# Performance work log

Hardware: AMD Instinct MI355X
Metric: run time of the kernel (lower is better)

## Reference

```python
import jax, jax.numpy as jnp
import numpy as np

N, E, F, H, C = 100000, 1600000, 128, 128, 40


def setup_inputs() -> dict:
    key = jax.random.key(0)
    ks = jax.random.split(key, 9)
    feat = jax.random.normal(ks[0], (N, F), dtype=jnp.float32)
    src = jax.random.randint(ks[1], (E,), 0, N, dtype=jnp.int32)
    dst = jax.random.randint(ks[2], (E,), 0, N, dtype=jnp.int32)
    def glorot(k, fan_in, fan_out):
        s = np.float32(np.sqrt(6.0 / (fan_in + fan_out)))
        return jax.random.uniform(k, (fan_in, fan_out), jnp.float32, -s, s)
    W0 = glorot(ks[3], F, H); b0 = jnp.zeros((H,), jnp.float32)
    W1 = glorot(ks[4], H, H); b1 = jnp.zeros((H,), jnp.float32)
    W2 = glorot(ks[5], H, C); b2 = jnp.zeros((C,), jnp.float32)
    return {"feat": feat, "src": src, "dst": dst,
            "W0": W0, "b0": b0, "W1": W1, "b1": b1, "W2": W2, "b2": b2}


def _graph_conv(h, src, dst, norm_out, norm_in, W, b):
    # DGL GraphConv, norm='both': out = D_in^{-1/2} A D_out^{-1/2} h W + b
    h = h * norm_out[:, None]          # scale by source out-degree
    h = h @ W                          # transform first (in_dim >= out_dim path)
    agg = jax.ops.segment_sum(h[src], dst, num_segments=N)  # scatter-add over edges
    return agg * norm_in[:, None] + b


def reference(feat, src, dst, W0, b0, W1, b1, W2, b2):
    ones_e = jnp.ones((E,), jnp.float32)
    deg_out = jax.ops.segment_sum(ones_e, src, num_segments=N)
    deg_in = jax.ops.segment_sum(ones_e, dst, num_segments=N)
    norm_out = jnp.where(deg_out > 0, jax.lax.rsqrt(jnp.maximum(deg_out, 1.0)), 0.0)
    norm_in = jnp.where(deg_in > 0, jax.lax.rsqrt(jnp.maximum(deg_in, 1.0)), 0.0)
    h = _graph_conv(feat, src, dst, norm_out, norm_in, W0, b0)
    h = jax.nn.relu(h)
    h = _graph_conv(h, src, dst, norm_out, norm_in, W1, b1)
    h = jax.nn.relu(h)
    h = _graph_conv(h, src, dst, norm_out, norm_in, W2, b2)
    return h
```

## Files before the change

### kernel.cpp

```cpp
#include <hip/hip_runtime.h>


#define KDIM 128
#define EPB 4096

typedef __attribute__((ext_vector_type(4))) float f32x4;
typedef __attribute__((ext_vector_type(8))) short short8;

__device__ __forceinline__ float bf2f(unsigned short u) {
    unsigned int x = ((unsigned int)u) << 16;
    return __builtin_bit_cast(float, x);
}
__device__ __forceinline__ unsigned short f2bf(float f) {
    unsigned int x = __builtin_bit_cast(unsigned int, f);
    unsigned int r = x + 0x7FFFu + ((x >> 16) & 1u);
    return (unsigned short)(r >> 16);
}

__global__ __launch_bounds__(256) void b0_count(const int* __restrict__ src,
                                                const int* __restrict__ dst,
                                                int* __restrict__ gcntA,
                                                int* __restrict__ gcntB, int E, int nb) {
    __shared__ int hA[512], hB[512];
    const int t = threadIdx.x;
    for (int b = t; b < nb; b += 256) { hA[b] = 0; hB[b] = 0; }
    __syncthreads();
    const int base = blockIdx.x * EPB;
#pragma unroll
    for (int i = 0; i < 16; ++i) {
        int e = base + i * 256 + t;
        if (e < E) {
            atomicAdd(&hA[dst[e] >> 8], 1);
            atomicAdd(&hB[src[e] >> 8], 1);
        }
    }
    __syncthreads();
    for (int b = t; b < nb; b += 256) {
        if (hA[b]) atomicAdd(&gcntA[b], hA[b]);
        if (hB[b]) atomicAdd(&gcntB[b], hB[b]);
    }
}

__global__ __launch_bounds__(512) void b0b_offsets(const int* __restrict__ gcntA,
                                                   const int* __restrict__ gcntB,
                                                   int* __restrict__ offA,
                                                   int* __restrict__ offB,
                                                   int* __restrict__ gcurA,
                                                   int* __restrict__ gcurB,
                                                   int* __restrict__ row_off,
                                                   int nb, int N, int E) {
    __shared__ int sm[512];
    const int t = threadIdx.x;
    int v = (t < nb) ? gcntA[t] : 0;
    sm[t] = v;
    __syncthreads();
    for (int o = 1; o < 512; o <<= 1) {
        int x = (t >= o) ? sm[t - o] : 0;
        __syncthreads();
        sm[t] += x;
        __syncthreads();
    }
    if (t < nb) { offA[t + 1] = sm[t]; gcurA[t] = sm[t] - v; }
    if (t == 0) { offA[0] = 0; row_off[N] = E; }
    __syncthreads();
    int vb = (t < nb) ? gcntB[t] : 0;
    sm[t] = vb;
    __syncthreads();
    for (int o = 1; o < 512; o <<= 1) {
        int x = (t >= o) ? sm[t - o] : 0;
        __syncthreads();
        sm[t] += x;
        __syncthreads();
    }
    if (t < nb) { offB[t + 1] = sm[t]; gcurB[t] = sm[t] - vb; }
    if (t == 0) offB[0] = 0;
}

__global__ __launch_bounds__(256) void b1_bin(const int* __restrict__ src,
                                              const int* __restrict__ dst,
                                              int* __restrict__ gcurA,
                                              int* __restrict__ gcurB,
                                              int* __restrict__ binA,
                                              int* __restrict__ binB, int E, int nb) {
    __shared__ int hA[512], hB[512];
    const int t = threadIdx.x;
    for (int b = t; b < nb; b += 256) { hA[b] = 0; hB[b] = 0; }
    __syncthreads();
    const int base = blockIdx.x * EPB;
    int se[16], de[16];
#pragma unroll
    for (int i = 0; i < 16; ++i) {
        int e = base + i * 256 + t;
        se[i] = -1; de[i] = 0;
        if (e < E) {
            se[i] = src[e]; de[i] = dst[e];
            atomicAdd(&hA[de[i] >> 8], 1);
            atomicAdd(&hB[se[i] >> 8], 1);
        }
    }
    __syncthreads();
    for (int b = t; b < nb; b += 256) {
        int c = hA[b];
        hA[b] = c ? atomicAdd(&gcurA[b], c) : 0;
        c = hB[b];
        hB[b] = c ? atomicAdd(&gcurB[b], c) : 0;
    }
    __syncthreads();
#pragma unroll
    for (int i = 0; i < 16; ++i) {
        if (se[i] >= 0) {
            int pA = atomicAdd(&hA[de[i] >> 8], 1);
            binA[pA] = se[i] | ((de[i] & 255) << 17);
            int pB = atomicAdd(&hB[se[i] >> 8], 1);
            binB[pB] = se[i] & 255;
        }
    }
}

__global__ __launch_bounds__(256) void b2_final(const int* __restrict__ binA,
                                                const int* __restrict__ binB,
                                                const int* __restrict__ offA,
                                                const int* __restrict__ offB,
                                                int* __restrict__ ssrc,
                                                int* __restrict__ row_off,
                                                float* __restrict__ norm_in,
                                                int* __restrict__ degO, int N) {
    __shared__ int h[256], cur[256];
    const int b = blockIdx.x, t = threadIdx.x;
    const int nA0 = offA[b], cntA = offA[b + 1] - nA0;
    const int nodes = min(256, N - b * 256);

    h[t] = 0;
    __syncthreads();
    for (int k = t; k < cntA; k += 256) atomicAdd(&h[binA[nA0 + k] >> 17], 1);
    __syncthreads();

    int v = h[t];
    cur[t] = v;
    __syncthreads();
    for (int o = 1; o < 256; o <<= 1) {
        int x = (t >= o) ? cur[t - o] : 0;
        __syncthreads();
        cur[t] += x;
        __syncthreads();
    }
    const int rbase = nA0 + (cur[t] - v);
    if (t < nodes) {
        row_off[b * 256 + t] = rbase;
        norm_in[b * 256 + t] = (v > 0) ? rsqrtf((float)v) : 0.0f;
    }
    __syncthreads();
    cur[t] = rbase;
    __syncthreads();

    for (int k = t; k < cntA; k += 256) {
        int val = binA[nA0 + k];
        int pos = atomicAdd(&cur[val >> 17], 1);
        ssrc[pos] = val & 0x1FFFF;
    }

    __syncthreads();
    h[t] = 0;
    __syncthreads();
    const int nB0 = offB[b], cntB = offB[b + 1] - nB0;
    for (int k = t; k < cntB; k += 256) atomicAdd(&h[binB[nB0 + k]], 1);
    __syncthreads();
    if (t < nodes) degO[b * 256 + t] = h[t];
}

__global__ __launch_bounds__(256) void prep_w(const float* __restrict__ W,
                                              unsigned int* __restrict__ Wtg) {
    int idx = blockIdx.x * 256 + threadIdx.x;
    if (idx < 8192) {
        int c = idx >> 6, kk = idx & 63;
        unsigned short lo = f2bf(W[(2 * kk) * 128 + c]);
        unsigned short hi = f2bf(W[(2 * kk + 1) * 128 + c]);
        Wtg[idx] = (unsigned)lo | ((unsigned)hi << 16);
    }
}

__global__ __launch_bounds__(256, 4) void gemm_mfma(const float* __restrict__ X,
                                                    const int* __restrict__ degO,
                                                    const unsigned int* __restrict__ Wtg,
                                                    unsigned short* __restrict__ Tb,
                                                    int ntiles, int gridWaves) {
    __shared__ unsigned int Wt[128 * 68];
    const int t = threadIdx.x;
    for (int idx = t; idx < 128 * 64; idx += 256) {
        int c = idx >> 6, kk = idx & 63;
        Wt[c * 68 + kk] = Wtg[idx];
    }
    __syncthreads();

    const int lane = t & 63;
    const int w = t >> 6;
    const int l15 = lane & 15;
    const int lh = lane >> 4;
    const unsigned short* Wts = reinterpret_cast<const unsigned short*>(Wt);
    const float4* X4 = reinterpret_cast<const float4*>(X);

    for (int tile = blockIdx.x * 4 + w; tile < ntiles; tile += gridWaves) {
        const int row = tile * 16 + l15;
        const int dv = degO[row];
        const float s = (dv > 0) ? rsqrtf((float)dv) : 0.0f;
        const float4* Xr = X4 + ((size_t)row * 32 + lh * 2);

        f32x4 acc[8];
#pragma unroll
        for (int ct = 0; ct < 8; ++ct) acc[ct] = f32x4{0.f, 0.f, 0.f, 0.f};

#pragma unroll
        for (int kc = 0; kc < 4; ++kc) {
            float4 a0 = Xr[kc * 8];
            float4 a1 = Xr[kc * 8 + 1];
            short8 af;
            af[0] = (short)f2bf(a0.x * s); af[1] = (short)f2bf(a0.y * s);
            af[2] = (short)f2bf(a0.z * s); af[3] = (short)f2bf(a0.w * s);
            af[4] = (short)f2bf(a1.x * s); af[5] = (short)f2bf(a1.y * s);
            af[6] = (short)f2bf(a1.z * s); af[7] = (short)f2bf(a1.w * s);
            const int k0 = kc * 32 + lh * 8;
#pragma unroll
            for (int ct = 0; ct < 8; ++ct) {
                short8 bf = *reinterpret_cast<const short8*>(&Wts[(ct * 16 + l15) * 136 + k0]);
                acc[ct] = __builtin_amdgcn_mfma_f32_16x16x32_bf16(af, bf, acc[ct], 0, 0, 0);
            }
        }

        const int rbase = tile * 16 + lh * 4;
#pragma unroll
        for (int ct = 0; ct < 8; ++ct) {
            const int col = ct * 16 + l15;
#pragma unroll
            for (int r = 0; r < 4; ++r)
                Tb[(size_t)(rbase + r) * 128 + col] = f2bf(acc[ct][r]);
        }
    }
}

__global__ __launch_bounds__(256) void agg_bf16(const unsigned short* __restrict__ Tb,
                                                const int* __restrict__ row_off,
                                                const int* __restrict__ ssrc,
                                                const float* __restrict__ norm_in,
                                                const float* __restrict__ bias,
                                                float* __restrict__ out, int n) {
    const int wid = (int)((blockIdx.x * blockDim.x + threadIdx.x) >> 6);
    const int lane = threadIdx.x & 63;
    if (wid >= n) return;
    const uint* T2 = reinterpret_cast<const uint*>(Tb);
    const int e0 = row_off[wid], e1 = row_off[wid + 1];
    float ax = 0.f, ay = 0.f;
    int e = e0;
    for (; e + 4 <= e1; e += 4) {
        int s0 = ssrc[e], s1 = ssrc[e + 1], s2 = ssrc[e + 2], s3 = ssrc[e + 3];
        uint v0 = T2[(size_t)s0 * 64 + lane];
        uint v1 = T2[(size_t)s1 * 64 + lane];
        uint v2 = T2[(size_t)s2 * 64 + lane];
        uint v3 = T2[(size_t)s3 * 64 + lane];
        ax += bf2f((unsigned short)v0) + bf2f((unsigned short)v1)
            + bf2f((unsigned short)v2) + bf2f((unsigned short)v3);
        ay += bf2f((unsigned short)(v0 >> 16)) + bf2f((unsigned short)(v1 >> 16))
            + bf2f((unsigned short)(v2 >> 16)) + bf2f((unsigned short)(v3 >> 16));
    }
    for (; e < e1; ++e) {
        uint v = T2[(size_t)ssrc[e] * 64 + lane];
        ax += bf2f((unsigned short)v);
        ay += bf2f((unsigned short)(v >> 16));
    }
    float ni = norm_in[wid];
    float2 b = reinterpret_cast<const float2*>(bias)[lane];
    float ox = fmaxf(ax * ni + b.x, 0.f);
    float oy = fmaxf(ay * ni + b.y, 0.f);
    reinterpret_cast<float2*>(out)[(size_t)wid * 64 + lane] = make_float2(ox, oy);
}

template <int M, int RPB, int CPT>
__global__ __launch_bounds__(256) void gemm_scaled(const float* __restrict__ X,
                                                   const int* __restrict__ degO,
                                                   const float* __restrict__ W,
                                                   float* __restrict__ T, int nrows) {
    constexpr int CG = M / CPT;
    static_assert(CG * (RPB / 2) == 256, "thread mapping");
    __shared__ float xs[KDIM][RPB + 1];
    __shared__ float ws[64][M];

    const int t = threadIdx.x;
    const int rowbase = blockIdx.x * RPB;

    {
        constexpr int NV = RPB * (KDIM / 4) / 256;
        const float4* X4 = reinterpret_cast<const float4*>(X);
#pragma unroll
        for (int i = 0; i < NV; ++i) {
            int idx = t + i * 256;
            int rl = idx >> 5;
            int kq = idx & 31;
            int row = rowbase + rl;
            float4 v = make_float4(0.f, 0.f, 0.f, 0.f);
            float s = 0.f;
            if (row < nrows) {
                v = X4[(size_t)row * 32 + kq];
                int dv = degO[row];
                s = (dv > 0) ? rsqrtf((float)dv) : 0.0f;
            }
            xs[4 * kq + 0][rl] = v.x * s;
            xs[4 * kq + 1][rl] = v.y * s;
            xs[4 * kq + 2][rl] = v.z * s;
            xs[4 * kq + 3][rl] = v.w * s;
        }
    }

    const int rg = t / CG, cg = t % CG;
    const int r0 = 2 * rg, cb = cg * CPT;
    float acc0[CPT] = {0.f}, acc1[CPT] = {0.f};

    for (int kc = 0; kc < 2; ++kc) {
        __syncthreads();
        {
            constexpr int TOT4 = 64 * M / 4;
            const float4* W4 = reinterpret_cast<const float4*>(W);
            for (int i = t; i < TOT4; i += 256) {
                int kk = i / (M / 4), m4 = i % (M / 4);
                float4 v = W4[(size_t)(kc * 64 + kk) * (M / 4) + m4];
                ws[kk][4 * m4 + 0] = v.x;
                ws[kk][4 * m4 + 1] = v.y;
                ws[kk][4 * m4 + 2] = v.z;
                ws[kk][4 * m4 + 3] = v.w;
            }
        }
        __syncthreads();
#pragma unroll 8
        for (int k = 0; k < 64; ++k) {
            float xv0 = xs[kc * 64 + k][r0];
            float xv1 = xs[kc * 64 + k][r0 + 1];
#pragma unroll
            for (int j = 0; j < CPT; ++j) {
                float wv = ws[k][cb + j];
                acc0[j] = fmaf(xv0, wv, acc0[j]);
                acc1[j] = fmaf(xv1, wv, acc1[j]);
            }
        }
    }

    int row0 = rowbase + r0;
    if (row0 < nrows) {
#pragma unroll
        for (int j = 0; j < CPT; ++j) T[(size_t)row0 * M + cb + j] = acc0[j];
    }
    if (row0 + 1 < nrows) {
#pragma unroll
        for (int j = 0; j < CPT; ++j) T[(size_t)(row0 + 1) * M + cb + j] = acc1[j];
    }
}

template <int M, bool RELU>
__global__ __launch_bounds__(256) void agg_kernel(const float* __restrict__ T,
                                                  const int* __restrict__ row_off,
                                                  const int* __restrict__ ssrc,
                                                  const float* __restrict__ norm_in,
                                                  const float* __restrict__ bias,
                                                  float* __restrict__ out, int n) {
    const int wid = (int)((blockIdx.x * blockDim.x + threadIdx.x) >> 6);
    const int lane = threadIdx.x & 63;
    if (wid >= n) return;
    constexpr int L = M / 2;
    const float2* T2 = reinterpret_cast<const float2*>(T);
    const int e0 = row_off[wid], e1 = row_off[wid + 1];
    if (lane < L) {
        float ax = 0.f, ay = 0.f;
        int e = e0;
        for (; e + 4 <= e1; e += 4) {
            int s0 = ssrc[e], s1 = ssrc[e + 1], s2 = ssrc[e + 2], s3 = ssrc[e + 3];
            float2 v0 = T2[s0 * L + lane];
            float2 v1 = T2[s1 * L + lane];
            float2 v2 = T2[s2 * L + lane];
            float2 v3 = T2[s3 * L + lane];
            ax += (v0.x + v1.x) + (v2.x + v3.x);
            ay += (v0.y + v1.y) + (v2.y + v3.y);
        }
        for (; e < e1; ++e) {
            int s = ssrc[e];
            float2 v = T2[s * L + lane];
            ax += v.x;
            ay += v.y;
        }
        float ni = norm_in[wid];
        float2 b = reinterpret_cast<const float2*>(bias)[lane];
        float ox = ax * ni + b.x;
        float oy = ay * ni + b.y;
        if (RELU) { ox = fmaxf(ox, 0.f); oy = fmaxf(oy, 0.f); }
        reinterpret_cast<float2*>(out)[(size_t)wid * L + lane] = make_float2(ox, oy);
    }
}

extern "C" void kernel_launch(void* const* d_in, const int* in_sizes, int n_in,
                              void* d_out, int out_size, void* d_ws, size_t ws_size,
                              hipStream_t stream) {
    const float* feat = (const float*)d_in[0];
    const int* src = (const int*)d_in[1];
    const int* dst = (const int*)d_in[2];
    const float* W0 = (const float*)d_in[3];
    const float* b0 = (const float*)d_in[4];
    const float* W1 = (const float*)d_in[5];
    const float* b1 = (const float*)d_in[6];
    const float* W2 = (const float*)d_in[7];
    const float* b2 = (const float*)d_in[8];
    float* outp = (float*)d_out;

    const int N = in_sizes[0] / KDIM;
    const int E = in_sizes[1];
    const int nb = (N + 255) >> 8;
    const int nblkE = (E + EPB - 1) / EPB;

    auto align = [](size_t x) { return (x + 255) & ~(size_t)255; };
    char* p = (char*)d_ws;
    int* degO      = (int*)p;    p += align((size_t)N * 4);
    float* norm_in = (float*)p;  p += align((size_t)N * 4);
    int* row_off   = (int*)p;    p += align((size_t)(N + 1) * 4);
    int* gcntA     = (int*)p;    p += 512 * 4;
    int* gcntB     = (int*)p;    p += 512 * 4;
    int* offA      = (int*)p;    p += align(513 * 4);
    int* offB      = (int*)p;    p += align(513 * 4);
    int* gcurA     = (int*)p;    p += align(512 * 4);
    int* gcurB     = (int*)p;    p += align(512 * 4);
    unsigned int* W0t = (unsigned int*)p;  p += align(8192 * 4);
    unsigned int* W1t = (unsigned int*)p;  p += align(8192 * 4);
    int* ssrc      = (int*)p;    p += align((size_t)E * 4);
    float* T       = (float*)p;  p += align((size_t)N * KDIM * 4);
    float* H       = (float*)p;  p += align((size_t)N * KDIM * 4);
    unsigned short* Tb = (unsigned short*)T;
    int* binA      = (int*)T;
    int* binB      = binA + E;
    (void)n_in; (void)out_size; (void)ws_size;

    const int aggBlocks = (int)(((size_t)N * 64 + 255) / 256);
    const int ntiles = N / 16;
    const int gBlocks = (ntiles + 3) / 4;
    const int gridWaves = gBlocks * 4;

    hipMemsetAsync(gcntA, 0, 1024 * 4, stream);

    prep_w<<<32, 256, 0, stream>>>(W0, W0t);
    prep_w<<<32, 256, 0, stream>>>(W1, W1t);

    b0_count<<<nblkE, 256, 0, stream>>>(src, dst, gcntA, gcntB, E, nb);
    b0b_offsets<<<1, 512, 0, stream>>>(gcntA, gcntB, offA, offB, gcurA, gcurB, row_off, nb, N, E);
    b1_bin<<<nblkE, 256, 0, stream>>>(src, dst, gcurA, gcurB, binA, binB, E, nb);
    b2_final<<<nb, 256, 0, stream>>>(binA, binB, offA, offB, ssrc, row_off, norm_in, degO, N);

    gemm_mfma<<<gBlocks, 256, 0, stream>>>(feat, degO, W0t, Tb, ntiles, gridWaves);
    agg_bf16<<<aggBlocks, 256, 0, stream>>>(Tb, row_off, ssrc, norm_in, b0, H, N);

    gemm_mfma<<<gBlocks, 256, 0, stream>>>(H, degO, W1t, Tb, ntiles, gridWaves);
    agg_bf16<<<aggBlocks, 256, 0, stream>>>(Tb, row_off, ssrc, norm_in, b1, H, N);

    gemm_scaled<40, 64, 5><<<(N + 63) / 64, 256, 0, stream>>>(H, degO, W2, T, N);
    agg_kernel<40, false><<<aggBlocks, 256, 0, stream>>>(T, row_off, ssrc, norm_in, b2, outp, N);
}
```

Before: 535.1 us.

## Use bf16 MFMA GEMM and packed-bf16 aggregation for final 40-class layer

Replaces the scalar fp32 GEMM of the last layer with the templated MFMA bf16 kernel, using 3 column tiles padded to 48 and a row stride of 64. The aggregation kernel becomes a bf16 gather in which four edges are processed in parallel per wave: 16-lane groups each take one edge and read 4 bf16 values per lane, then a shuffle reduction combines them. This is meant to halve the gather bytes and raise lane utilisation compared with the old float2 gather that used only 20 of 64 lanes. The cost is lower precision in the final layer's intermediate values.

```diff
diff --git a/kernel.cpp b/kernel.cpp
--- a/kernel.cpp
+++ b/kernel.cpp
@@ -168,25 +168,31 @@
     if (t < nodes) degO[b * 256 + t] = h[t];
 }
 
+template <int M, int CPAD>
 __global__ __launch_bounds__(256) void prep_w(const float* __restrict__ W,
                                               unsigned int* __restrict__ Wtg) {
     int idx = blockIdx.x * 256 + threadIdx.x;
-    if (idx < 8192) {
+    if (idx < CPAD * 64) {
         int c = idx >> 6, kk = idx & 63;
-        unsigned short lo = f2bf(W[(2 * kk) * 128 + c]);
-        unsigned short hi = f2bf(W[(2 * kk + 1) * 128 + c]);
-        Wtg[idx] = (unsigned)lo | ((unsigned)hi << 16);
-    }
-}
-
+        unsigned int pk = 0;
+        if (c < M) {
+            unsigned short lo = f2bf(W[(2 * kk) * M + c]);
+            unsigned short hi = f2bf(W[(2 * kk + 1) * M + c]);
+            pk = (unsigned)lo | ((unsigned)hi << 16);
+        }
+        Wtg[idx] = pk;
+    }
+}
+
+template <int CT, int OSTRIDE>
 __global__ __launch_bounds__(256, 4) void gemm_mfma(const float* __restrict__ X,
                                                     const int* __restrict__ degO,
                                                     const unsigned int* __restrict__ Wtg,
                                                     unsigned short* __restrict__ Tb,
                                                     int ntiles, int gridWaves) {
-    __shared__ unsigned int Wt[128 * 68];
+    __shared__ unsigned int Wt[CT * 16 * 68];
     const int t = threadIdx.x;
-    for (int idx = t; idx < 128 * 64; idx += 256) {
+    for (int idx = t; idx < CT * 16 * 64; idx += 256) {
         int c = idx >> 6, kk = idx & 63;
         Wt[c * 68 + kk] = Wtg[idx];
     }
@@ -205,9 +211,9 @@
         const float s = (dv > 0) ? rsqrtf((float)dv) : 0.0f;
         const float4* Xr = X4 + ((size_t)row * 32 + lh * 2);
 
-        f32x4 acc[8];
-#pragma unroll
-        for (int ct = 0; ct < 8; ++ct) acc[ct] = f32x4{0.f, 0.f, 0.f, 0.f};
+        f32x4 acc[CT];
+#pragma unroll
+        for (int ct = 0; ct < CT; ++ct) acc[ct] = f32x4{0.f, 0.f, 0.f, 0.f};
 
 #pragma unroll
         for (int kc = 0; kc < 4; ++kc) {
@@ -220,7 +226,7 @@
             af[6] = (short)f2bf(a1.z * s); af[7] = (short)f2bf(a1.w * s);
             const int k0 = kc * 32 + lh * 8;
 #pragma unroll
-            for (int ct = 0; ct < 8; ++ct) {
+            for (int ct = 0; ct < CT; ++ct) {
                 short8 bf = *reinterpret_cast<const short8*>(&Wts[(ct * 16 + l15) * 136 + k0]);
                 acc[ct] = __builtin_amdgcn_mfma_f32_16x16x32_bf16(af, bf, acc[ct], 0, 0, 0);
             }
@@ -228,11 +234,11 @@
 
         const int rbase = tile * 16 + lh * 4;
 #pragma unroll
-        for (int ct = 0; ct < 8; ++ct) {
+        for (int ct = 0; ct < CT; ++ct) {
             const int col = ct * 16 + l15;
 #pragma unroll
             for (int r = 0; r < 4; ++r)
-                Tb[(size_t)(rbase + r) * 128 + col] = f2bf(acc[ct][r]);
+                Tb[(size_t)(rbase + r) * OSTRIDE + col] = f2bf(acc[ct][r]);
         }
     }
 }
@@ -273,122 +279,77 @@
     reinterpret_cast<float2*>(out)[(size_t)wid * 64 + lane] = make_float2(ox, oy);
 }
 
-template <int M, int RPB, int CPT>
-__global__ __launch_bounds__(256) void gemm_scaled(const float* __restrict__ X,
-                                                   const int* __restrict__ degO,
-                                                   const float* __restrict__ W,
-                                                   float* __restrict__ T, int nrows) {
-    constexpr int CG = M / CPT;
-    static_assert(CG * (RPB / 2) == 256, "thread mapping");
-    __shared__ float xs[KDIM][RPB + 1];
-    __shared__ float ws[64][M];
-
-    const int t = threadIdx.x;
-    const int rowbase = blockIdx.x * RPB;
-
-    {
-        constexpr int NV = RPB * (KDIM / 4) / 256;
-        const float4* X4 = reinterpret_cast<const float4*>(X);
-#pragma unroll
-        for (int i = 0; i < NV; ++i) {
-            int idx = t + i * 256;
-            int rl = idx >> 5;
-            int kq = idx & 31;
-            int row = rowbase + rl;
-            float4 v = make_float4(0.f, 0.f, 0.f, 0.f);
-            float s = 0.f;
-            if (row < nrows) {
-                v = X4[(size_t)row * 32 + kq];
-                int dv = degO[row];
-                s = (dv > 0) ? rsqrtf((float)dv) : 0.0f;
-            }
-            xs[4 * kq + 0][rl] = v.x * s;
-            xs[4 * kq + 1][rl] = v.y * s;
-            xs[4 * kq + 2][rl] = v.z * s;
-            xs[4 * kq + 3][rl] = v.w * s;
-        }
-    }
-
-    const int rg = t / CG, cg = t % CG;
-    const int r0 = 2 * rg, cb = cg * CPT;
-    float acc0[CPT] = {0.f}, acc1[CPT] = {0.f};
-
-    for (int kc = 0; kc < 2; ++kc) {
-        __syncthreads();
-        {
-            constexpr int TOT4 = 64 * M / 4;
-            const float4* W4 = reinterpret_cast<const float4*>(W);
-            for (int i = t; i < TOT4; i += 256) {
-                int kk = i / (M / 4), m4 = i % (M / 4);
-                float4 v = W4[(size_t)(kc * 64 + kk) * (M / 4) + m4];
-                ws[kk][4 * m4 + 0] = v.x;
-                ws[kk][4 * m4 + 1] = v.y;
-                ws[kk][4 * m4 + 2] = v.z;
-                ws[kk][4 * m4 + 3] = v.w;
-            }
-        }
-        __syncthreads();
-#pragma unroll 8
-        for (int k = 0; k < 64; ++k) {
-            float xv0 = xs[kc * 64 + k][r0];
-            float xv1 = xs[kc * 64 + k][r0 + 1];
-#pragma unroll
-            for (int j = 0; j < CPT; ++j) {
-                float wv = ws[k][cb + j];
-                acc0[j] = fmaf(xv0, wv, acc0[j]);
-                acc1[j] = fmaf(xv1, wv, acc1[j]);
-            }
-        }
-    }
-
-    int row0 = rowbase + r0;
-    if (row0 < nrows) {
-#pragma unroll
-        for (int j = 0; j < CPT; ++j) T[(size_t)row0 * M + cb + j] = acc0[j];
-    }
-    if (row0 + 1 < nrows) {
-#pragma unroll
-        for (int j = 0; j < CPT; ++j) T[(size_t)(row0 + 1) * M + cb + j] = acc1[j];
-    }
-}
-
-template <int M, bool RELU>
-__global__ __launch_bounds__(256) void agg_kernel(const float* __restrict__ T,
-                                                  const int* __restrict__ row_off,
-                                                  const int* __restrict__ ssrc,
-                                                  const float* __restrict__ norm_in,
-                                                  const float* __restrict__ bias,
-                                                  float* __restrict__ out, int n) {
+__global__ __launch_bounds__(256) void agg_f3(const unsigned short* __restrict__ T3,
+                                              const int* __restrict__ row_off,
+                                              const int* __restrict__ ssrc,
+                                              const float* __restrict__ norm_in,
+                                              const float* __restrict__ bias,
+                                              float* __restrict__ out, int n) {
     const int wid = (int)((blockIdx.x * blockDim.x + threadIdx.x) >> 6);
     const int lane = threadIdx.x & 63;
     if (wid >= n) return;
-    constexpr int L = M / 2;
-    const float2* T2 = reinterpret_cast<const float2*>(T);
-    const int e0 = row_off[wid], e1 = row_off[wid + 1];
-    if (lane < L) {
-        float ax = 0.f, ay = 0.f;
-        int e = e0;
-        for (; e + 4 <= e1; e += 4) {
-            int s0 = ssrc[e], s1 = ssrc[e + 1], s2 = ssrc[e + 2], s3 = ssrc[e + 3];
-            float2 v0 = T2[s0 * L + lane];
-            float2 v1 = T2[s1 * L + lane];
-            float2 v2 = T2[s2 * L + lane];
-            float2 v3 = T2[s3 * L + lane];
-            ax += (v0.x + v1.x) + (v2.x + v3.x);
-            ay += (v0.y + v1.y) + (v2.y + v3.y);
-        }
-        for (; e < e1; ++e) {
-            int s = ssrc[e];
-            float2 v = T2[s * L + lane];
-            ax += v.x;
-            ay += v.y;
-        }
-        float ni = norm_in[wid];
-        float2 b = reinterpret_cast<const float2*>(bias)[lane];
-        float ox = ax * ni + b.x;
-        float oy = ay * ni + b.y;
-        if (RELU) { ox = fmaxf(ox, 0.f); oy = fmaxf(oy, 0.f); }
-        reinterpret_cast<float2*>(out)[(size_t)wid * L + lane] = make_float2(ox, oy);
+    const int g = lane >> 4;
+    const int j = lane & 15;
+    const bool act = (j < 10);
+
+    const int e0 = row_off[wid];
+    const int cnt = row_off[wid + 1] - e0;
+    const float ni = norm_in[wid];
+    const int niter = (cnt + 3) >> 2;
+
+    const uint2* T3q = reinterpret_cast<const uint2*>(T3);
+
+    float a0 = 0.f, a1 = 0.f, a2 = 0.f, a3 = 0.f;
+    float c0 = 0.f, c1 = 0.f, c2 = 0.f, c3 = 0.f;
+    int it = 0;
+    for (; it + 2 <= niter; it += 2) {
+        const int i0 = it * 4 + g, i1 = i0 + 4;
+        if (act && i0 < cnt) {
+            int s = ssrc[e0 + i0];
+            uint2 q = T3q[(size_t)s * 16 + j];
+            a0 += bf2f((unsigned short)q.x);
+            a1 += bf2f((unsigned short)(q.x >> 16));
+            a2 += bf2f((unsigned short)q.y);
+            a3 += bf2f((unsigned short)(q.y >> 16));
+        }
+        if (act && i1 < cnt) {
+            int s = ssrc[e0 + i1];
+            uint2 q = T3q[(size_t)s * 16 + j];
+            c0 += bf2f((unsigned short)q.x);
+            c1 += bf2f((unsigned short)(q.x >> 16));
+            c2 += bf2f((unsigned short)q.y);
+            c3 += bf2f((unsigned short)(q.y >> 16));
+        }
+    }
+    if (it < niter) {
+        const int i0 = it * 4 + g;
+        if (act && i0 < cnt) {
+            int s = ssrc[e0 + i0];
+            uint2 q = T3q[(size_t)s * 16 + j];
+            a0 += bf2f((unsigned short)q.x);
+            a1 += bf2f((unsigned short)(q.x >> 16));
+            a2 += bf2f((unsigned short)q.y);
+            a3 += bf2f((unsigned short)(q.y >> 16));
+        }
+    }
+    a0 += c0; a1 += c1; a2 += c2; a3 += c3;
+
+#pragma unroll
+    for (int m = 16; m < 64; m <<= 1) {
+        a0 += __shfl_xor(a0, m, 64);
+        a1 += __shfl_xor(a1, m, 64);
+        a2 += __shfl_xor(a2, m, 64);
+        a3 += __shfl_xor(a3, m, 64);
+    }
+
+    if (g == 0 && act) {
+        float4 bb = reinterpret_cast<const float4*>(bias)[j];
+        float4 o;
+        o.x = a0 * ni + bb.x;
+        o.y = a1 * ni + bb.y;
+        o.z = a2 * ni + bb.z;
+        o.w = a3 * ni + bb.w;
+        reinterpret_cast<float4*>(out)[(size_t)wid * 10 + j] = o;
     }
 }
 
@@ -424,10 +385,12 @@
     int* gcurB     = (int*)p;    p += align(512 * 4);
     unsigned int* W0t = (unsigned int*)p;  p += align(8192 * 4);
     unsigned int* W1t = (unsigned int*)p;  p += align(8192 * 4);
+    unsigned int* W2t = (unsigned int*)p;  p += align(3072 * 4);
     int* ssrc      = (int*)p;    p += align((size_t)E * 4);
     float* T       = (float*)p;  p += align((size_t)N * KDIM * 4);
     float* H       = (float*)p;  p += align((size_t)N * KDIM * 4);
     unsigned short* Tb = (unsigned short*)T;
+    unsigned short* T3 = (unsigned short*)T;
     int* binA      = (int*)T;
     int* binB      = binA + E;
     (void)n_in; (void)out_size; (void)ws_size;
@@ -439,20 +402,21 @@
 
     hipMemsetAsync(gcntA, 0, 1024 * 4, stream);
 
-    prep_w<<<32, 256, 0, stream>>>(W0, W0t);
-    prep_w<<<32, 256, 0, stream>>>(W1, W1t);
+    prep_w<128, 128><<<32, 256, 0, stream>>>(W0, W0t);
+    prep_w<128, 128><<<32, 256, 0, stream>>>(W1, W1t);
+    prep_w<40, 48><<<12, 256, 0, stream>>>(W2, W2t);
 
     b0_count<<<nblkE, 256, 0, stream>>>(src, dst, gcntA, gcntB, E, nb);
     b0b_offsets<<<1, 512, 0, stream>>>(gcntA, gcntB, offA, offB, gcurA, gcurB, row_off, nb, N, E);
     b1_bin<<<nblkE, 256, 0, stream>>>(src, dst, gcurA, gcurB, binA, binB, E, nb);
     b2_final<<<nb, 256, 0, stream>>>(binA, binB, offA, offB, ssrc, row_off, norm_in, degO, N);
 
-    gemm_mfma<<<gBlocks, 256, 0, stream>>>(feat, degO, W0t, Tb, ntiles, gridWaves);
+    gemm_mfma<8, 128><<<gBlocks, 256, 0, stream>>>(feat, degO, W0t, Tb, ntiles, gridWaves);
     agg_bf16<<<aggBlocks, 256, 0, stream>>>(Tb, row_off, ssrc, norm_in, b0, H, N);
 
-    gemm_mfma<<<gBlocks, 256, 0, stream>>>(H, degO, W1t, Tb, ntiles, gridWaves);
+    gemm_mfma<8, 128><<<gBlocks, 256, 0, stream>>>(H, degO, W1t, Tb, ntiles, gridWaves);
     agg_bf16<<<aggBlocks, 256, 0, stream>>>(Tb, row_off, ssrc, norm_in, b1, H, N);
 
-    gemm_scaled<40, 64, 5><<<(N + 63) / 64, 256, 0, stream>>>(H, degO, W2, T, N);
-    agg_kernel<40, false><<<aggBlocks, 256, 0, stream>>>(T, row_off, ssrc, norm_in, b2, outp, N);
-}
+    gemm_mfma<3, 64><<<gBlocks, 256, 0, stream>>>(H, degO, W2t, T3, ntiles, gridWaves);
+    agg_f3<<<aggBlocks, 256, 0, stream>>>(T3, row_off, ssrc, norm_in, b2, outp, N);
+}
```

New measurement: 500.1 us. 1.07x faster.
